# Performance work log

Hardware: AMD Instinct MI355X
Metric: run time of the kernel (lower is better)

## Reference

```python
import jax, jax.numpy as jnp
import numpy as np

MESH = 4194304

def setup_inputs() -> dict:
    key = jax.random.key(0)
    k1, k2 = jax.random.split(key)
    theta_t = jax.random.normal(k1, (MESH - 1,), dtype=jnp.float32) * 0.01
    state = jax.random.normal(k2, (MESH, 2), dtype=jnp.float32)
    # SSH eigenstates are unit vectors
    state = state / jnp.linalg.norm(state, axis=-1, keepdims=True)
    return {"theta_t": theta_t, "state": state}

def reference(theta_t, state):
    M = state.shape[0]
    # --- deformation: deformed[0]=state[0]; deformed[i+1] = R(theta[i]) @ state[i+1]
    c, s = jnp.cos(theta_t), jnp.sin(theta_t)            # (M-1,)
    sx, sy = state[1:, 0], state[1:, 1]
    rot = jnp.stack([c * sx - s * sy, s * sx + c * sy], axis=-1)  # (M-1, 2)
    deformed = jnp.concatenate([state[:1], rot], axis=0)          # (M, 2)
    # --- neighbor overlaps (periodic): dots[i] = d_i . d_{i+1}, dots[M-1] = d_{M-1} . d_0
    dots = jnp.sum(deformed * jnp.roll(deformed, -1, axis=0), axis=-1)  # (M,)
    vols = jnp.sqrt(jnp.abs(1.0 - jnp.abs(dots) ** 2))                   # (M,)
    loss_v = jnp.sum(vols)
    loss_s = jnp.sum(vols ** 2)
    # --- dirichlet / SO(2) smoothness loss; average_length uses vol_loss.item() (stop-grad)
    avg_len = jnp.abs(jax.lax.stop_gradient(loss_v) / M)
    sim = jnp.exp(-vols / avg_len)                       # used for i = 0 .. M-2
    # note: original wrap-around similarity has NO sqrt (faithful to source)
    sim_last = jnp.exp(-(1.0 - jnp.abs(dots[-1]) ** 2) / avg_len)
    loss_so2 = (jnp.abs(theta_t[0]) * sim[0]
                + jnp.abs(theta_t[-1]) * sim_last
                + jnp.sum(jnp.abs(theta_t[:-1] - theta_t[1:]) * sim[1:M - 1]))
    # total loss with ratio = ratio_s = 1.0
    return loss_v + loss_so2 + loss_s
```

## Files before the change

### kernel.cpp

```cpp
#include <hip/hip_runtime.h>
#include <math.h>

#define MESH 4194304
#define NBLOCKS 2048
#define NTHREADS 256
#define QPG 2

__device__ __forceinline__ float2 rot2(float t, float x, float y) {
  float s, c;
  __sincosf(t, &s, &c);
  return make_float2(c * x - s * y, s * x + c * y);
}

__device__ __forceinline__ float block_reduce(float v, float* red) {
  #pragma unroll
  for (int off = 32; off > 0; off >>= 1) v += __shfl_down(v, off);
  const int lane = threadIdx.x & 63, wid = threadIdx.x >> 6;
  if (lane == 0) red[wid] = v;
  __syncthreads();
  return red[0] + red[1] + red[2] + red[3];
}

template <bool PASS_C>
__global__ void pass_kernel(const float* __restrict__ theta,
                            const float* __restrict__ statef,
                            const float* __restrict__ inv_avg_p,
                            float2* __restrict__ pv,
                            float* __restrict__ pl) {
  const int tid = threadIdx.x;
  const int lane = tid & 63, wid = tid >> 6;
  const int wbase = (blockIdx.x * 4 + wid) << 9;

  float4 tf[QPG], sA[QPG], sB[QPG];
  #pragma unroll
  for (int g = 0; g < QPG; ++g) {
    const int e0 = wbase + (g << 8) + (lane << 2);
    if (e0 != MESH - 4) {
      tf[g] = *(const float4*)(theta + e0);
    } else {
      tf[g] = make_float4(theta[e0], theta[e0 + 1], theta[e0 + 2], 0.f);
    }
    sA[g] = *(const float4*)(statef + 2 * e0);
    sB[g] = *(const float4*)(statef + 2 * e0 + 4);
  }
  float th_carry = 0.f;
  if (lane == 0 && wbase > 0) th_carry = theta[wbase - 1];
  float2 s_carry = make_float2(0.f, 0.f);
  if (lane == 63) {
    const int en = (wbase + 512 == MESH) ? 0 : wbase + 512;
    s_carry = make_float2(statef[2 * en], statef[2 * en + 1]);
  }
  const float inv_avg = PASS_C ? *inv_avg_p : 0.f;

  float acc0 = 0.f, acc1 = 0.f;
  #pragma unroll
  for (int g = 0; g < QPG; ++g) {
    const int e0 = wbase + (g << 8) + (lane << 2);
    const float prevw = (g == 0) ? th_carry : __shfl(tf[g - 1].w, 63);
    float th0 = __shfl_up(tf[g].w, 1);
    if (lane == 0) th0 = prevw;
    const float bx = (g + 1 < QPG) ? __shfl(sA[g + 1].x, 0) : s_carry.x;
    const float by = (g + 1 < QPG) ? __shfl(sA[g + 1].y, 0) : s_carry.y;
    float nx = __shfl_down(sA[g].x, 1);
    float ny = __shfl_down(sA[g].y, 1);
    if (lane == 63) { nx = bx; ny = by; }

    const float2 d0 = rot2(th0,     sA[g].x, sA[g].y);
    const float2 d1 = rot2(tf[g].x, sA[g].z, sA[g].w);
    const float2 d2 = rot2(tf[g].y, sB[g].x, sB[g].y);
    const float2 d3 = rot2(tf[g].z, sB[g].z, sB[g].w);
    const float2 d4 = rot2(tf[g].w, nx, ny);

    const float dots[4] = {d0.x * d1.x + d0.y * d1.y, d1.x * d2.x + d1.y * d2.y,
                           d2.x * d3.x + d2.y * d3.y, d3.x * d4.x + d3.y * d4.y};
    if (!PASS_C) {
      #pragma unroll
      for (int j = 0; j < 4; ++j) {
        const float v2 = fabsf(1.f - dots[j] * dots[j]);
        acc0 += sqrtf(v2);
        acc1 += v2;
      }
    } else {
      const float thseq[5] = {th0, tf[g].x, tf[g].y, tf[g].z, tf[g].w};
      #pragma unroll
      for (int j = 0; j < 4; ++j) {
        const float v2s = 1.f - dots[j] * dots[j];
        const float w = fabsf(thseq[j] - thseq[j + 1]);
        const float earg = (e0 == MESH - 4 && j == 3) ? v2s : sqrtf(fabsf(v2s));
        acc0 += w * __expf(-earg * inv_avg);
      }
    }
  }

  __shared__ float red1[4], red2[4];
  if (!PASS_C) {
    const float b0 = block_reduce(acc0, red1);
    const float b1 = block_reduce(acc1, red2);
    if (tid == 0) pv[blockIdx.x] = make_float2(b0, b1);
  } else {
    const float b0 = block_reduce(acc0, red1);
    if (tid == 0) pl[blockIdx.x] = b0;
  }
}

__global__ void reduceA_kernel(const float2* __restrict__ pv,
                               double* __restrict__ acc,
                               float* __restrict__ inv_avg) {
  double lv = 0.0, ls = 0.0;
  for (int i = threadIdx.x; i < NBLOCKS; i += 1024) {
    const float2 p = pv[i];
    lv += (double)p.x;
    ls += (double)p.y;
  }
  #pragma unroll
  for (int off = 32; off > 0; off >>= 1) {
    lv += __shfl_down(lv, off);
    ls += __shfl_down(ls, off);
  }
  __shared__ double s1[16], s2[16];
  const int lane = threadIdx.x & 63, wid = threadIdx.x >> 6;
  if (lane == 0) { s1[wid] = lv; s2[wid] = ls; }
  __syncthreads();
  if (threadIdx.x == 0) {
    double tlv = 0.0, tls = 0.0;
    #pragma unroll
    for (int w = 0; w < 16; ++w) { tlv += s1[w]; tls += s2[w]; }
    acc[0] = tlv + tls;
    *inv_avg = (float)((double)MESH / fabs(tlv));
  }
}

__global__ void reduceC_kernel(const float* __restrict__ pl,
                               const double* __restrict__ acc,
                               float* __restrict__ out) {
  double lso = 0.0;
  for (int i = threadIdx.x; i < NBLOCKS; i += 1024) lso += (double)pl[i];
  #pragma unroll
  for (int off = 32; off > 0; off >>= 1) lso += __shfl_down(lso, off);
  __shared__ double s1[16];
  const int lane = threadIdx.x & 63, wid = threadIdx.x >> 6;
  if (lane == 0) s1[wid] = lso;
  __syncthreads();
  if (threadIdx.x == 0) {
    double t = 0.0;
    #pragma unroll
    for (int w = 0; w < 16; ++w) t += s1[w];
    out[0] = (float)(acc[0] + t);
  }
}

extern "C" void kernel_launch(void* const* d_in, const int* in_sizes, int n_in,
                              void* d_out, int out_size, void* d_ws, size_t ws_size,
                              hipStream_t stream) {
  const float* theta  = (const float*)d_in[0];
  const float* statef = (const float*)d_in[1];
  float* out = (float*)d_out;

  char* ws = (char*)d_ws;
  float2* pv = (float2*)ws;
  float* pl = (float*)(ws + 16384);
  double* acc = (double*)(ws + 24576);
  float* inv_avg = (float*)(ws + 24576 + 16);

  pass_kernel<false><<<NBLOCKS, NTHREADS, 0, stream>>>(theta, statef, inv_avg, pv, pl);
  reduceA_kernel<<<1, 1024, 0, stream>>>(pv, acc, inv_avg);
  pass_kernel<true><<<NBLOCKS, NTHREADS, 0, stream>>>(theta, statef, inv_avg, pv, pl);
  reduceC_kernel<<<1, 1024, 0, stream>>>(pl, acc, out);
}
```

Baseline: 98.00 us.

## Fuse both passes into one kernel with a grid-wide spin barrier

Merges the two streaming passes and the middle reduction into one persistent kernel. Each block keeps its per-element vols and theta differences in registers, publishes its partial sums via atomic release stores, and block 0 gathers all partials and broadcasts the inverse average length through a flag that every block spins on. This avoids re-reading theta and state from memory and removes a kernel launch, at the cost of requiring all 2048 blocks to be co-resident (hence the launch bounds of 8 blocks per CU), which risks deadlock if occupancy falls short. A small init kernel resets the sentinels on every call.

```diff
diff --git a/kernel.cpp b/kernel.cpp
--- a/kernel.cpp
+++ b/kernel.cpp
@@ -5,6 +5,9 @@
 #define NBLOCKS 2048
 #define NTHREADS 256
 #define QPG 2
+
+#define PV_SENTINEL 0xFFFFFFFFFFFFFFFFull
+#define FLAG_SENTINEL 0xFFFFFFFFu
 
 __device__ __forceinline__ float2 rot2(float t, float x, float y) {
   float s, c;
@@ -21,12 +24,20 @@
   return red[0] + red[1] + red[2] + red[3];
 }
 
-template <bool PASS_C>
-__global__ void pass_kernel(const float* __restrict__ theta,
-                            const float* __restrict__ statef,
-                            const float* __restrict__ inv_avg_p,
-                            float2* __restrict__ pv,
-                            float* __restrict__ pl) {
+__global__ void init_kernel(unsigned long long* __restrict__ pv,
+                            unsigned* __restrict__ flag) {
+  #pragma unroll
+  for (int k = 0; k < 8; ++k) pv[threadIdx.x * 8 + k] = PV_SENTINEL;
+  if (threadIdx.x == 0) *flag = FLAG_SENTINEL;
+}
+
+__global__ __launch_bounds__(NTHREADS, 8)
+void fused_kernel(const float* __restrict__ theta,
+                  const float* __restrict__ statef,
+                  unsigned long long* __restrict__ pv,
+                  unsigned* __restrict__ flag,
+                  double* __restrict__ accsum,
+                  float* __restrict__ pl) {
   const int tid = threadIdx.x;
   const int lane = tid & 63, wid = tid >> 6;
   const int wbase = (blockIdx.x * 4 + wid) << 9;
@@ -50,9 +61,9 @@
     const int en = (wbase + 512 == MESH) ? 0 : wbase + 512;
     s_carry = make_float2(statef[2 * en], statef[2 * en + 1]);
   }
-  const float inv_avg = PASS_C ? *inv_avg_p : 0.f;
 
-  float acc0 = 0.f, acc1 = 0.f;
+  float earg8[4 * QPG], w8[4 * QPG];
+  float lv = 0.f, ls = 0.f;
   #pragma unroll
   for (int g = 0; g < QPG; ++g) {
     const int e0 = wbase + (g << 8) + (lane << 2);
@@ -73,66 +84,81 @@
 
     const float dots[4] = {d0.x * d1.x + d0.y * d1.y, d1.x * d2.x + d1.y * d2.y,
                            d2.x * d3.x + d2.y * d3.y, d3.x * d4.x + d3.y * d4.y};
-    if (!PASS_C) {
-      #pragma unroll
-      for (int j = 0; j < 4; ++j) {
-        const float v2 = fabsf(1.f - dots[j] * dots[j]);
-        acc0 += sqrtf(v2);
-        acc1 += v2;
-      }
-    } else {
-      const float thseq[5] = {th0, tf[g].x, tf[g].y, tf[g].z, tf[g].w};
-      #pragma unroll
-      for (int j = 0; j < 4; ++j) {
-        const float v2s = 1.f - dots[j] * dots[j];
-        const float w = fabsf(thseq[j] - thseq[j + 1]);
-        const float earg = (e0 == MESH - 4 && j == 3) ? v2s : sqrtf(fabsf(v2s));
-        acc0 += w * __expf(-earg * inv_avg);
-      }
+    const float thseq[5] = {th0, tf[g].x, tf[g].y, tf[g].z, tf[g].w};
+    #pragma unroll
+    for (int j = 0; j < 4; ++j) {
+      const float v2s = 1.f - dots[j] * dots[j];
+      const float v2 = fabsf(v2s);
+      const float vol = sqrtf(v2);
+      lv += vol;
+      ls += v2;
+      earg8[g * 4 + j] = (e0 == MESH - 4 && j == 3) ? v2s : vol;
+      w8[g * 4 + j] = fabsf(thseq[j] - thseq[j + 1]);
     }
   }
 
   __shared__ float red1[4], red2[4];
-  if (!PASS_C) {
-    const float b0 = block_reduce(acc0, red1);
-    const float b1 = block_reduce(acc1, red2);
-    if (tid == 0) pv[blockIdx.x] = make_float2(b0, b1);
-  } else {
-    const float b0 = block_reduce(acc0, red1);
-    if (tid == 0) pl[blockIdx.x] = b0;
+  const float blv = block_reduce(lv, red1);
+  const float bls = block_reduce(ls, red2);
+  if (tid == 0) {
+    const unsigned long long packed =
+        (unsigned long long)__float_as_uint(blv) |
+        ((unsigned long long)__float_as_uint(bls) << 32);
+    __hip_atomic_store(&pv[blockIdx.x], packed, __ATOMIC_RELEASE, __HIP_MEMORY_SCOPE_AGENT);
   }
+
+  if (blockIdx.x == 0) {
+    double mlv = 0.0, mls = 0.0;
+    #pragma unroll
+    for (int k = 0; k < 8; ++k) {
+      const int idx = tid * 8 + k;
+      unsigned long long v;
+      while ((v = __hip_atomic_load(&pv[idx], __ATOMIC_RELAXED, __HIP_MEMORY_SCOPE_AGENT))
+             == PV_SENTINEL) {
+        __builtin_amdgcn_s_sleep(4);
+      }
+      mlv += (double)__uint_as_float((unsigned)v);
+      mls += (double)__uint_as_float((unsigned)(v >> 32));
+    }
+    #pragma unroll
+    for (int off = 32; off > 0; off >>= 1) {
+      mlv += __shfl_down(mlv, off);
+      mls += __shfl_down(mls, off);
+    }
+    __shared__ double d1[4], d2[4];
+    if (lane == 0) { d1[wid] = mlv; d2[wid] = mls; }
+    __syncthreads();
+    if (tid == 0) {
+      const double tlv = d1[0] + d1[1] + d1[2] + d1[3];
+      const double tls = d2[0] + d2[1] + d2[2] + d2[3];
+      accsum[0] = tlv + tls;
+      const float inv = (float)((double)MESH / fabs(tlv));
+      __hip_atomic_store(flag, __float_as_uint(inv), __ATOMIC_RELEASE, __HIP_MEMORY_SCOPE_AGENT);
+    }
+  }
+
+  __shared__ float s_inv;
+  if (tid == 0) {
+    unsigned f;
+    while ((f = __hip_atomic_load(flag, __ATOMIC_RELAXED, __HIP_MEMORY_SCOPE_AGENT))
+           == FLAG_SENTINEL) {
+      __builtin_amdgcn_s_sleep(16);
+    }
+    s_inv = __uint_as_float(f);
+  }
+  __syncthreads();
+
+  const float inv_avg = s_inv;
+  float lso = 0.f;
+  #pragma unroll
+  for (int k = 0; k < 4 * QPG; ++k) lso += w8[k] * __expf(-earg8[k] * inv_avg);
+  const float blso = block_reduce(lso, red1);
+  if (tid == 0) pl[blockIdx.x] = blso;
 }
 
-__global__ void reduceA_kernel(const float2* __restrict__ pv,
-                               double* __restrict__ acc,
-                               float* __restrict__ inv_avg) {
-  double lv = 0.0, ls = 0.0;
-  for (int i = threadIdx.x; i < NBLOCKS; i += 1024) {
-    const float2 p = pv[i];
-    lv += (double)p.x;
-    ls += (double)p.y;
-  }
-  #pragma unroll
-  for (int off = 32; off > 0; off >>= 1) {
-    lv += __shfl_down(lv, off);
-    ls += __shfl_down(ls, off);
-  }
-  __shared__ double s1[16], s2[16];
-  const int lane = threadIdx.x & 63, wid = threadIdx.x >> 6;
-  if (lane == 0) { s1[wid] = lv; s2[wid] = ls; }
-  __syncthreads();
-  if (threadIdx.x == 0) {
-    double tlv = 0.0, tls = 0.0;
-    #pragma unroll
-    for (int w = 0; w < 16; ++w) { tlv += s1[w]; tls += s2[w]; }
-    acc[0] = tlv + tls;
-    *inv_avg = (float)((double)MESH / fabs(tlv));
-  }
-}
-
-__global__ void reduceC_kernel(const float* __restrict__ pl,
-                               const double* __restrict__ acc,
-                               float* __restrict__ out) {
+__global__ void final_kernel(const float* __restrict__ pl,
+                             const double* __restrict__ accsum,
+                             float* __restrict__ out) {
   double lso = 0.0;
   for (int i = threadIdx.x; i < NBLOCKS; i += 1024) lso += (double)pl[i];
   #pragma unroll
@@ -145,7 +171,7 @@
     double t = 0.0;
     #pragma unroll
     for (int w = 0; w < 16; ++w) t += s1[w];
-    out[0] = (float)(acc[0] + t);
+    out[0] = (float)(accsum[0] + t);
   }
 }
 
@@ -157,13 +183,12 @@
   float* out = (float*)d_out;
 
   char* ws = (char*)d_ws;
-  float2* pv = (float2*)ws;
+  unsigned long long* pv = (unsigned long long*)ws;
   float* pl = (float*)(ws + 16384);
-  double* acc = (double*)(ws + 24576);
-  float* inv_avg = (float*)(ws + 24576 + 16);
+  double* accsum = (double*)(ws + 24576);
+  unsigned* flag = (unsigned*)(ws + 24576 + 128);
 
-  pass_kernel<false><<<NBLOCKS, NTHREADS, 0, stream>>>(theta, statef, inv_avg, pv, pl);
-  reduceA_kernel<<<1, 1024, 0, stream>>>(pv, acc, inv_avg);
-  pass_kernel<true><<<NBLOCKS, NTHREADS, 0, stream>>>(theta, statef, inv_avg, pv, pl);
-  reduceC_kernel<<<1, 1024, 0, stream>>>(pl, acc, out);
+  init_kernel<<<1, NTHREADS, 0, stream>>>(pv, flag);
+  fused_kernel<<<NBLOCKS, NTHREADS, 0, stream>>>(theta, statef, pv, flag, accsum, pl);
+  final_kernel<<<1, 1024, 0, stream>>>(pl, accsum, out);
 }
```

After: 136.2 us. 1.39x slower.

## Materialize per-edge vol and theta-diff pairs to avoid recomputing rotations in second pass

Applied to the files above, without the earlier changes.

The first pass now stores, for every edge, the vol value (or the unsquare-rooted wrap-around term) and the absolute theta difference into a workspace buffer. A new lightweight second pass streams those pairs and applies the exponential weighting, instead of reloading theta and state and recomputing the sincos rotations and dot products. The small reduction kernels also drop from 1024 to 256 threads. The trade-off is more total memory traffic: a 32 MB write plus a 32 MB read replace a 48 MB re-read. It also needs a much larger workspace.

```diff
diff --git a/kernel.cpp b/kernel.cpp
--- a/kernel.cpp
+++ b/kernel.cpp
@@ -21,12 +21,10 @@
   return red[0] + red[1] + red[2] + red[3];
 }
 
-template <bool PASS_C>
-__global__ void pass_kernel(const float* __restrict__ theta,
-                            const float* __restrict__ statef,
-                            const float* __restrict__ inv_avg_p,
-                            float2* __restrict__ pv,
-                            float* __restrict__ pl) {
+__global__ void passA_kernel(const float* __restrict__ theta,
+                             const float* __restrict__ statef,
+                             float2* __restrict__ pairs,
+                             float2* __restrict__ pv) {
   const int tid = threadIdx.x;
   const int lane = tid & 63, wid = tid >> 6;
   const int wbase = (blockIdx.x * 4 + wid) << 9;
@@ -50,9 +48,8 @@
     const int en = (wbase + 512 == MESH) ? 0 : wbase + 512;
     s_carry = make_float2(statef[2 * en], statef[2 * en + 1]);
   }
-  const float inv_avg = PASS_C ? *inv_avg_p : 0.f;
 
-  float acc0 = 0.f, acc1 = 0.f;
+  float lv = 0.f, ls = 0.f;
   #pragma unroll
   for (int g = 0; g < QPG; ++g) {
     const int e0 = wbase + (g << 8) + (lane << 2);
@@ -73,41 +70,34 @@
 
     const float dots[4] = {d0.x * d1.x + d0.y * d1.y, d1.x * d2.x + d1.y * d2.y,
                            d2.x * d3.x + d2.y * d3.y, d3.x * d4.x + d3.y * d4.y};
-    if (!PASS_C) {
-      #pragma unroll
-      for (int j = 0; j < 4; ++j) {
-        const float v2 = fabsf(1.f - dots[j] * dots[j]);
-        acc0 += sqrtf(v2);
-        acc1 += v2;
-      }
-    } else {
-      const float thseq[5] = {th0, tf[g].x, tf[g].y, tf[g].z, tf[g].w};
-      #pragma unroll
-      for (int j = 0; j < 4; ++j) {
-        const float v2s = 1.f - dots[j] * dots[j];
-        const float w = fabsf(thseq[j] - thseq[j + 1]);
-        const float earg = (e0 == MESH - 4 && j == 3) ? v2s : sqrtf(fabsf(v2s));
-        acc0 += w * __expf(-earg * inv_avg);
-      }
+    const float thseq[5] = {th0, tf[g].x, tf[g].y, tf[g].z, tf[g].w};
+    float ew[8];
+    #pragma unroll
+    for (int j = 0; j < 4; ++j) {
+      const float v2s = 1.f - dots[j] * dots[j];
+      const float v2 = fabsf(v2s);
+      const float vol = sqrtf(v2);
+      lv += vol;
+      ls += v2;
+      ew[2 * j]     = (e0 == MESH - 4 && j == 3) ? v2s : vol;
+      ew[2 * j + 1] = fabsf(thseq[j] - thseq[j + 1]);
     }
+    float4* dst = (float4*)(pairs + e0);
+    dst[0] = make_float4(ew[0], ew[1], ew[2], ew[3]);
+    dst[1] = make_float4(ew[4], ew[5], ew[6], ew[7]);
   }
 
   __shared__ float red1[4], red2[4];
-  if (!PASS_C) {
-    const float b0 = block_reduce(acc0, red1);
-    const float b1 = block_reduce(acc1, red2);
-    if (tid == 0) pv[blockIdx.x] = make_float2(b0, b1);
-  } else {
-    const float b0 = block_reduce(acc0, red1);
-    if (tid == 0) pl[blockIdx.x] = b0;
-  }
+  const float blv = block_reduce(lv, red1);
+  const float bls = block_reduce(ls, red2);
+  if (tid == 0) pv[blockIdx.x] = make_float2(blv, bls);
 }
 
 __global__ void reduceA_kernel(const float2* __restrict__ pv,
-                               double* __restrict__ acc,
+                               double* __restrict__ accsum,
                                float* __restrict__ inv_avg) {
   double lv = 0.0, ls = 0.0;
-  for (int i = threadIdx.x; i < NBLOCKS; i += 1024) {
+  for (int i = threadIdx.x; i < NBLOCKS; i += NTHREADS) {
     const float2 p = pv[i];
     lv += (double)p.x;
     ls += (double)p.y;
@@ -117,36 +107,49 @@
     lv += __shfl_down(lv, off);
     ls += __shfl_down(ls, off);
   }
-  __shared__ double s1[16], s2[16];
+  __shared__ double s1[4], s2[4];
   const int lane = threadIdx.x & 63, wid = threadIdx.x >> 6;
   if (lane == 0) { s1[wid] = lv; s2[wid] = ls; }
   __syncthreads();
   if (threadIdx.x == 0) {
-    double tlv = 0.0, tls = 0.0;
-    #pragma unroll
-    for (int w = 0; w < 16; ++w) { tlv += s1[w]; tls += s2[w]; }
-    acc[0] = tlv + tls;
+    const double tlv = s1[0] + s1[1] + s1[2] + s1[3];
+    const double tls = s2[0] + s2[1] + s2[2] + s2[3];
+    accsum[0] = tlv + tls;
     *inv_avg = (float)((double)MESH / fabs(tlv));
   }
 }
 
-__global__ void reduceC_kernel(const float* __restrict__ pl,
-                               const double* __restrict__ acc,
-                               float* __restrict__ out) {
+__global__ void passC_kernel(const float4* __restrict__ pairs4,
+                             const float* __restrict__ inv_avg_p,
+                             float* __restrict__ pl) {
+  const float ninv = -(*inv_avg_p);
+  const int base = blockIdx.x * (NTHREADS * 4) + threadIdx.x;
+  float4 p[4];
+  #pragma unroll
+  for (int k = 0; k < 4; ++k) p[k] = pairs4[base + k * NTHREADS];
+  float lso = 0.f;
+  #pragma unroll
+  for (int k = 0; k < 4; ++k) {
+    lso += p[k].y * __expf(p[k].x * ninv);
+    lso += p[k].w * __expf(p[k].z * ninv);
+  }
+  __shared__ float red1[4];
+  const float b = block_reduce(lso, red1);
+  if (threadIdx.x == 0) pl[blockIdx.x] = b;
+}
+
+__global__ void final_kernel(const float* __restrict__ pl,
+                             const double* __restrict__ accsum,
+                             float* __restrict__ out) {
   double lso = 0.0;
-  for (int i = threadIdx.x; i < NBLOCKS; i += 1024) lso += (double)pl[i];
+  for (int i = threadIdx.x; i < NBLOCKS; i += NTHREADS) lso += (double)pl[i];
   #pragma unroll
   for (int off = 32; off > 0; off >>= 1) lso += __shfl_down(lso, off);
-  __shared__ double s1[16];
+  __shared__ double s1[4];
   const int lane = threadIdx.x & 63, wid = threadIdx.x >> 6;
   if (lane == 0) s1[wid] = lso;
   __syncthreads();
-  if (threadIdx.x == 0) {
-    double t = 0.0;
-    #pragma unroll
-    for (int w = 0; w < 16; ++w) t += s1[w];
-    out[0] = (float)(acc[0] + t);
-  }
+  if (threadIdx.x == 0) out[0] = (float)(accsum[0] + s1[0] + s1[1] + s1[2] + s1[3]);
 }
 
 extern "C" void kernel_launch(void* const* d_in, const int* in_sizes, int n_in,
@@ -157,13 +160,14 @@
   float* out = (float*)d_out;
 
   char* ws = (char*)d_ws;
-  float2* pv = (float2*)ws;
-  float* pl = (float*)(ws + 16384);
-  double* acc = (double*)(ws + 24576);
-  float* inv_avg = (float*)(ws + 24576 + 16);
+  float2* pairs = (float2*)ws;
+  float2* pv = (float2*)(ws + (size_t)MESH * 8);
+  float* pl = (float*)(ws + (size_t)MESH * 8 + 16384);
+  double* accsum = (double*)(ws + (size_t)MESH * 8 + 16384 + 8192);
+  float* inv_avg = (float*)(ws + (size_t)MESH * 8 + 16384 + 8192 + 64);
 
-  pass_kernel<false><<<NBLOCKS, NTHREADS, 0, stream>>>(theta, statef, inv_avg, pv, pl);
-  reduceA_kernel<<<1, 1024, 0, stream>>>(pv, acc, inv_avg);
-  pass_kernel<true><<<NBLOCKS, NTHREADS, 0, stream>>>(theta, statef, inv_avg, pv, pl);
-  reduceC_kernel<<<1, 1024, 0, stream>>>(pl, acc, out);
+  passA_kernel<<<NBLOCKS, NTHREADS, 0, stream>>>(theta, statef, pairs, pv);
+  reduceA_kernel<<<1, NTHREADS, 0, stream>>>(pv, accsum, inv_avg);
+  passC_kernel<<<NBLOCKS, NTHREADS, 0, stream>>>((const float4*)pairs, inv_avg, pl);
+  final_kernel<<<1, NTHREADS, 0, stream>>>(pl, accsum, out);
 }
```

Result: no change. 99.93 us (+2.0%).
